# Optimization experiments

Measured on AMD Instinct MI355X. Metric: run time of the kernel, lower is better.

## Reference

```python
import jax, jax.numpy as jnp
import numpy as np

B, S, D = 2, 2048, 7168
R, H, VD = 1024, 16, 128
QK_HD = R // H            # 64, per-head latent q/k dim
SCALE = float(np.sqrt(D // H))  # self.scale = d_heads ** 0.5 = sqrt(448)


def setup_inputs() -> dict:
    key = jax.random.key(0)
    ks = jax.random.split(key, 6)
    return {
        "x":   jax.random.normal(ks[0], (B, S, D), dtype=jnp.float32),
        "Wq":  jax.random.normal(ks[1], (R, D), dtype=jnp.float32) * 0.02,
        "Wkv": jax.random.normal(ks[2], (R, D), dtype=jnp.float32) * 0.02,
        "Wvb": jax.random.normal(ks[3], (H * VD, R), dtype=jnp.float32) * 0.02,
        "Wo":  jax.random.normal(ks[4], (D, H * VD), dtype=jnp.float32) * 0.02,
        "bo":  jnp.zeros((D,), dtype=jnp.float32),
    }


def reference(x, Wq, Wkv, Wvb, Wo, bo):
    b, s, d = x.shape
    # low-rank compressed projections (torch Linear: y = x @ W.T)
    q_lat  = x @ Wq.T            # [B,S,R] compressed query
    kv_lat = x @ Wkv.T           # [B,S,R] compressed KV latent (shared K)
    q = q_lat.reshape(b, s, H, QK_HD)    # [B,S,H,64]
    k = kv_lat.reshape(b, s, H, QK_HD)   # [B,S,H,64]
    # up-project values from latent
    v = (kv_lat @ Wvb.T).reshape(b, s, H, VD)  # [B,S,H,128]
    # scaled causal attention in latent head space
    scores = jnp.einsum("bqhd,bkhd->bhqk", q, k) / SCALE  # [B,H,S,S]
    causal = jnp.tril(jnp.ones((s, s), dtype=bool))
    scores = jnp.where(causal, scores, jnp.finfo(scores.dtype).min)
    attn = jax.nn.softmax(scores, axis=-1)
    out = jnp.einsum("bhqk,bkhd->bqhd", attn, v).reshape(b, s, H * VD)
    return out @ Wo.T + bo       # [B,S,D]
```

## Files before the change

kernel.cpp:

```cpp
#include <hip/hip_runtime.h>
#include <hip/hip_bf16.h>

typedef __bf16 bf16_t;
typedef __attribute__((ext_vector_type(8))) __bf16 bf16x8;
typedef __attribute__((ext_vector_type(4))) __bf16 bf16x4;
typedef __attribute__((ext_vector_type(4))) float f32x4;

#define B_ 2
#define S_ 2048
#define D_ 7168
#define R_ 1024
#define H_ 16
#define VD_ 128
#define MROWS 4096
#define NQKV 2048
#define HVD 2048

__device__ __forceinline__ void gload_lds16(const bf16_t* g, bf16_t* l) {
    __builtin_amdgcn_global_load_lds(
        (const __attribute__((address_space(1))) unsigned int*)(g),
        (__attribute__((address_space(3))) unsigned int*)(l),
        16, 0, 0);
}

__global__ __launch_bounds__(256)
void cvt_fused(const float* __restrict__ x,  const float* __restrict__ Wq,
               const float* __restrict__ Wkv, const float* __restrict__ Wvb,
               const float* __restrict__ Wo,
               bf16_t* __restrict__ xb, bf16_t* __restrict__ Wqkv_b,
               bf16_t* __restrict__ Wvb_b, bf16_t* __restrict__ Wo_b,
               float inv_scale)
{
    const long c = ((long)blockIdx.x * 256 + threadIdx.x);
    const long e = c * 8;
    const float* src; bf16_t* dst; long off; float scale = 1.0f;
    if (e < 29360128L) {
        src = x;   dst = xb;              off = e;
    } else if (e < 36700160L) {
        src = Wq;  dst = Wqkv_b;          off = e - 29360128L; scale = inv_scale;
    } else if (e < 44040192L) {
        src = Wkv; dst = Wqkv_b + 7340032; off = e - 36700160L;
    } else if (e < 46137344L) {
        src = Wvb; dst = Wvb_b;           off = e - 44040192L;
    } else {
        src = Wo;  dst = Wo_b;            off = e - 46137344L;
    }
    f32x4 v0 = *(const f32x4*)(src + off);
    f32x4 v1 = *(const f32x4*)(src + off + 4);
    bf16x8 o;
    o[0] = (bf16_t)(v0[0] * scale); o[1] = (bf16_t)(v0[1] * scale);
    o[2] = (bf16_t)(v0[2] * scale); o[3] = (bf16_t)(v0[3] * scale);
    o[4] = (bf16_t)(v1[0] * scale); o[5] = (bf16_t)(v1[1] * scale);
    o[6] = (bf16_t)(v1[2] * scale); o[7] = (bf16_t)(v1[3] * scale);
    *(bf16x8*)(dst + off) = o;
}

template<int OUTF32>
__global__ __launch_bounds__(256)
void gemm_bt(const bf16_t* __restrict__ A, int lda,
             const bf16_t* __restrict__ Bt, int ldb,
             void* __restrict__ Cv, int ldc,
             const float* __restrict__ bias, int K)
{
    __shared__ __align__(16) bf16_t As[2][128 * 64];
    __shared__ __align__(16) bf16_t Bs[2][128 * 64];
    const int tid  = threadIdx.x;
    const int lane = tid & 63;
    const int wave = tid >> 6;
    const int tileM = blockIdx.y * 128;
    const int tileN = blockIdx.x * 128;
    const int wr = (wave >> 1) * 64;
    const int wc = (wave & 1) * 64;
    const int r  = lane & 15;
    const int kq = lane >> 4;

    const bf16_t* Ag = A  + (size_t)tileM * lda;
    const bf16_t* Bg = Bt + (size_t)tileN * ldb;

    int srow[4], scol[4], slin[4];
    #pragma unroll
    for (int i = 0; i < 4; ++i) {
        slin[i] = (i * 256 + tid) * 8;
        srow[i] = slin[i] >> 6;
        scol[i] = (slin[i] & 63) ^ ((srow[i] & 7) << 3);
    }

    #define ISSUE_TILE(buf, k0)                                                  \
        {                                                                        \
            _Pragma("unroll")                                                    \
            for (int i = 0; i < 4; ++i) {                                        \
                gload_lds16(Ag + (size_t)srow[i] * lda + (k0) + scol[i], As[buf] + slin[i]); \
                gload_lds16(Bg + (size_t)srow[i] * ldb + (k0) + scol[i], Bs[buf] + slin[i]); \
            }                                                                    \
        }

    f32x4 acc[4][4] = {};
    const int nt = K >> 6;

    ISSUE_TILE(0, 0)
    ISSUE_TILE(1, 64)
    asm volatile("s_waitcnt vmcnt(8)" ::: "memory");
    __builtin_amdgcn_s_barrier();
    __builtin_amdgcn_sched_barrier(0);

    for (int t = 0; t < nt; ++t) {
        const int cur = t & 1;
        const bf16_t* Ab = As[cur];
        const bf16_t* Bb = Bs[cur];

        bf16x8 af[4][2], bfr[4][2];
        #pragma unroll
        for (int m = 0; m < 4; ++m)
            #pragma unroll
            for (int kk = 0; kk < 2; ++kk) {
                const int e = (wr + m * 16 + r) * 64 + kk * 32 + kq * 8;
                af[m][kk] = *(const bf16x8*)(Ab + (e ^ ((r & 7) << 3)));
            }
        #pragma unroll
        for (int n = 0; n < 4; ++n)
            #pragma unroll
            for (int kk = 0; kk < 2; ++kk) {
                const int e = (wc + n * 16 + r) * 64 + kk * 32 + kq * 8;
                bfr[n][kk] = *(const bf16x8*)(Bb + (e ^ ((r & 7) << 3)));
            }
        __builtin_amdgcn_s_setprio(1);
        #pragma unroll
        for (int kk = 0; kk < 2; ++kk)
            #pragma unroll
            for (int m = 0; m < 4; ++m)
                #pragma unroll
                for (int n = 0; n < 4; ++n)
                    acc[m][n] = __builtin_amdgcn_mfma_f32_16x16x32_bf16(af[m][kk], bfr[n][kk], acc[m][n], 0, 0, 0);
        __builtin_amdgcn_s_setprio(0);

        __builtin_amdgcn_s_barrier();
        __builtin_amdgcn_sched_barrier(0);
        if (t + 2 < nt) {
            ISSUE_TILE(cur, (t + 2) << 6)
            asm volatile("s_waitcnt vmcnt(8)" ::: "memory");
        } else {
            asm volatile("s_waitcnt vmcnt(0)" ::: "memory");
        }
        __builtin_amdgcn_s_barrier();
        __builtin_amdgcn_sched_barrier(0);
    }
    #undef ISSUE_TILE

    const int orow = tileM + wr + kq * 4;
    const int ocol = tileN + wc + r;
    if (OUTF32) {
        float* C = (float*)Cv;
        #pragma unroll
        for (int n = 0; n < 4; ++n) {
            float bv = bias[ocol + n * 16];
            #pragma unroll
            for (int m = 0; m < 4; ++m)
                #pragma unroll
                for (int j = 0; j < 4; ++j)
                    C[(size_t)(orow + m * 16 + j) * ldc + ocol + n * 16] = acc[m][n][j] + bv;
        }
    } else {
        bf16_t* C = (bf16_t*)Cv;
        #pragma unroll
        for (int m = 0; m < 4; ++m)
            #pragma unroll
            for (int n = 0; n < 4; ++n)
                #pragma unroll
                for (int j = 0; j < 4; ++j)
                    C[(size_t)(orow + m * 16 + j) * ldc + ocol + n * 16] = (bf16_t)acc[m][n][j];
    }
}

template<int OUTF32>
__global__ __launch_bounds__(512, 2)
void gemm_bt256(const bf16_t* __restrict__ A, int lda,
                const bf16_t* __restrict__ Bt, int ldb,
                void* __restrict__ Cv, int ldc,
                const float* __restrict__ bias, int K)
{
    __shared__ __align__(16) bf16_t As[2][256 * 64];
    __shared__ __align__(16) bf16_t Bs[2][256 * 64];
    const int tid  = threadIdx.x;
    const int lane = tid & 63;
    const int wave = tid >> 6;
    const int wm = wave >> 2;
    const int wn = wave & 3;
    const int tileM = blockIdx.y * 256;
    const int tileN = blockIdx.x * 256;
    const int r  = lane & 15;
    const int kq = lane >> 4;

    const bf16_t* Ag = A  + (size_t)tileM * lda;
    const bf16_t* Bg = Bt + (size_t)tileN * ldb;

    int srow[4], scol[4], slin[4];
    #pragma unroll
    for (int i = 0; i < 4; ++i) {
        slin[i] = (i * 512 + tid) * 8;
        srow[i] = slin[i] >> 6;
        scol[i] = (slin[i] & 63) ^ ((srow[i] & 7) << 3);
    }

    #define ISSUE_TILE2(buf, k0)                                                 \
        {                                                                        \
            _Pragma("unroll")                                                    \
            for (int i = 0; i < 4; ++i) {                                        \
                gload_lds16(Ag + (size_t)srow[i] * lda + (k0) + scol[i], As[buf] + slin[i]); \
                gload_lds16(Bg + (size_t)srow[i] * ldb + (k0) + scol[i], Bs[buf] + slin[i]); \
            }                                                                    \
        }

    f32x4 acc[8][4] = {};
    const int nt = K >> 6;

    ISSUE_TILE2(0, 0)
    ISSUE_TILE2(1, 64)
    asm volatile("s_waitcnt vmcnt(8)" ::: "memory");
    __builtin_amdgcn_s_barrier();
    __builtin_amdgcn_sched_barrier(0);

    for (int t = 0; t < nt; ++t) {
        const int cur = t & 1;
        const bf16_t* Ab = As[cur];
        const bf16_t* Bb = Bs[cur];

        {
            bf16x8 af[8], bfr[4];
            #pragma unroll
            for (int m = 0; m < 8; ++m) {
                const int e = (wm * 128 + m * 16 + r) * 64 + kq * 8;
                af[m] = *(const bf16x8*)(Ab + (e ^ ((r & 7) << 3)));
            }
            #pragma unroll
            for (int n = 0; n < 4; ++n) {
                const int e = (wn * 64 + n * 16 + r) * 64 + kq * 8;
                bfr[n] = *(const bf16x8*)(Bb + (e ^ ((r & 7) << 3)));
            }
            __builtin_amdgcn_s_setprio(1);
            #pragma unroll
            for (int m = 0; m < 8; ++m)
                #pragma unroll
                for (int n = 0; n < 4; ++n)
                    acc[m][n] = __builtin_amdgcn_mfma_f32_16x16x32_bf16(af[m], bfr[n], acc[m][n], 0, 0, 0);
            __builtin_amdgcn_s_setprio(0);
        }
        bf16x8 af1[8], bf1[4];
        #pragma unroll
        for (int m = 0; m < 8; ++m) {
            const int e = (wm * 128 + m * 16 + r) * 64 + 32 + kq * 8;
            af1[m] = *(const bf16x8*)(Ab + (e ^ ((r & 7) << 3)));
        }
        #pragma unroll
        for (int n = 0; n < 4; ++n) {
            const int e = (wn * 64 + n * 16 + r) * 64 + 32 + kq * 8;
            bf1[n] = *(const bf16x8*)(Bb + (e ^ ((r & 7) << 3)));
        }
        asm volatile("s_waitcnt lgkmcnt(0)" ::: "memory");
        __builtin_amdgcn_sched_barrier(0);
        __builtin_amdgcn_s_barrier();

        if (t + 2 < nt) { ISSUE_TILE2(cur, (t + 2) << 6) }

        __builtin_amdgcn_s_setprio(1);
        #pragma unroll
        for (int m = 0; m < 8; ++m)
            #pragma unroll
            for (int n = 0; n < 4; ++n)
                acc[m][n] = __builtin_amdgcn_mfma_f32_16x16x32_bf16(af1[m], bf1[n], acc[m][n], 0, 0, 0);
        __builtin_amdgcn_s_setprio(0);

        if (t + 2 < nt) asm volatile("s_waitcnt vmcnt(8)" ::: "memory");
        else            asm volatile("s_waitcnt vmcnt(0)" ::: "memory");
        __builtin_amdgcn_sched_barrier(0);
        __builtin_amdgcn_s_barrier();
        __builtin_amdgcn_sched_barrier(0);
    }
    #undef ISSUE_TILE2

    const int orow = tileM + wm * 128 + kq * 4;
    const int ocol = tileN + wn * 64 + r;
    if (OUTF32) {
        float* C = (float*)Cv;
        #pragma unroll
        for (int n = 0; n < 4; ++n) {
            float bv = bias[ocol + n * 16];
            #pragma unroll
            for (int m = 0; m < 8; ++m)
                #pragma unroll
                for (int j = 0; j < 4; ++j)
                    C[(size_t)(orow + m * 16 + j) * ldc + ocol + n * 16] = acc[m][n][j] + bv;
        }
    } else {
        bf16_t* C = (bf16_t*)Cv;
        #pragma unroll
        for (int m = 0; m < 8; ++m)
            #pragma unroll
            for (int n = 0; n < 4; ++n)
                #pragma unroll
                for (int j = 0; j < 4; ++j)
                    C[(size_t)(orow + m * 16 + j) * ldc + ocol + n * 16] = (bf16_t)acc[m][n][j];
    }
}

__device__ __forceinline__ void attn_qtile(
    const bf16_t* __restrict__ Q, const bf16_t* __restrict__ Kp,
    const bf16_t* __restrict__ Vp, bf16_t* __restrict__ Op,
    bf16_t* __restrict__ P_lds, int qbase, int lane)
{
    const int r  = lane & 15;
    const int kq = lane >> 4;

    bf16x8 qf[2][2];
    #pragma unroll
    for (int m = 0; m < 2; ++m)
        #pragma unroll
        for (int kk = 0; kk < 2; ++kk)
            qf[m][kk] = *(const bf16x8*)(Q + (size_t)(qbase + m * 16 + r) * NQKV + kk * 32 + kq * 8);

    f32x4 o[2][8] = {};
    float mst[2][4], lst[2][4];
    #pragma unroll
    for (int m = 0; m < 2; ++m)
        #pragma unroll
        for (int j = 0; j < 4; ++j) { mst[m][j] = -INFINITY; lst[m][j] = 0.0f; }

    const int nfull  = qbase >> 6;
    const int ntiles = (qbase + 95) >> 6;

    for (int t = 0; t < ntiles; ++t) {
        const int kvb = t * 64;
        f32x4 s[2][4] = {};
        #pragma unroll
        for (int n = 0; n < 4; ++n) {
            bf16x8 kf0 = *(const bf16x8*)(Kp + (size_t)(kvb + n * 16 + r) * NQKV + kq * 8);
            bf16x8 kf1 = *(const bf16x8*)(Kp + (size_t)(kvb + n * 16 + r) * NQKV + 32 + kq * 8);
            #pragma unroll
            for (int m = 0; m < 2; ++m) {
                s[m][n] = __builtin_amdgcn_mfma_f32_16x16x32_bf16(qf[m][0], kf0, s[m][n], 0, 0, 0);
                s[m][n] = __builtin_amdgcn_mfma_f32_16x16x32_bf16(qf[m][1], kf1, s[m][n], 0, 0, 0);
            }
        }
        if (t >= nfull) {
            #pragma unroll
            for (int m = 0; m < 2; ++m)
                #pragma unroll
                for (int n = 0; n < 4; ++n)
                    #pragma unroll
                    for (int j = 0; j < 4; ++j) {
                        int kc = kvb + n * 16 + r;
                        int qr = qbase + m * 16 + kq * 4 + j;
                        if (kc > qr) s[m][n][j] = -1e30f;
                    }
        }
        float mx[2][4];
        #pragma unroll
        for (int m = 0; m < 2; ++m)
            #pragma unroll
            for (int j = 0; j < 4; ++j) {
                float v = fmaxf(fmaxf(s[m][0][j], s[m][1][j]), fmaxf(s[m][2][j], s[m][3][j]));
                #pragma unroll
                for (int d = 1; d < 16; d <<= 1) v = fmaxf(v, __shfl_xor(v, d, 64));
                mx[m][j] = v;
            }
        bool need = false;
        #pragma unroll
        for (int m = 0; m < 2; ++m)
            #pragma unroll
            for (int j = 0; j < 4; ++j) need |= (mx[m][j] > mst[m][j] + 8.0f);
        if (__ballot(need)) {
            #pragma unroll
            for (int m = 0; m < 2; ++m)
                #pragma unroll
                for (int j = 0; j < 4; ++j) {
                    float mnew  = fmaxf(mst[m][j], mx[m][j]);
                    float alpha = __expf(mst[m][j] - mnew);
                    lst[m][j] *= alpha;
                    mst[m][j]  = mnew;
                    #pragma unroll
                    for (int n = 0; n < 8; ++n) o[m][n][j] *= alpha;
                }
        }
        #pragma unroll
        for (int m = 0; m < 2; ++m)
            #pragma unroll
            for (int j = 0; j < 4; ++j) {
                float rs = 0.0f;
                const int row = m * 16 + kq * 4 + j;
                #pragma unroll
                for (int n = 0; n < 4; ++n) {
                    float pv = __expf(s[m][n][j] - mst[m][j]);
                    rs += pv;
                    const int c = (n * 16 + r) ^ ((row & 7) << 3);
                    P_lds[row * 64 + c] = (bf16_t)pv;
                }
                #pragma unroll
                for (int d = 1; d < 16; d <<= 1) rs += __shfl_xor(rs, d, 64);
                lst[m][j] += rs;
            }
        __syncthreads();
        bf16x8 pf[2][2];
        #pragma unroll
        for (int m = 0; m < 2; ++m)
            #pragma unroll
            for (int kk = 0; kk < 2; ++kk) {
                const int e = (m * 16 + r) * 64 + kk * 32 + kq * 8;
                pf[m][kk] = *(const bf16x8*)(P_lds + (e ^ ((r & 7) << 3)));
            }
        #pragma unroll
        for (int n = 0; n < 8; ++n) {
            #pragma unroll
            for (int kk = 0; kk < 2; ++kk) {
                bf16x8 vf = *(const bf16x8*)(Vp + (size_t)(n * 16 + r) * MROWS + kvb + kk * 32 + kq * 8);
                #pragma unroll
                for (int m = 0; m < 2; ++m)
                    o[m][n] = __builtin_amdgcn_mfma_f32_16x16x32_bf16(pf[m][kk], vf, o[m][n], 0, 0, 0);
            }
        }
        __syncthreads();
    }

    #pragma unroll
    for (int m = 0; m < 2; ++m)
        #pragma unroll
        for (int j = 0; j < 4; ++j) {
            float inv = 1.0f / lst[m][j];
            int row = m * 16 + kq * 4 + j;
            #pragma unroll
            for (int n = 0; n < 8; ++n)
                Op[(size_t)(qbase + row) * HVD + n * 16 + r] = (bf16_t)(o[m][n][j] * inv);
        }
}

__global__ __launch_bounds__(64)
void attn_kernel(const bf16_t* __restrict__ qkv, const bf16_t* __restrict__ Vt,
                 bf16_t* __restrict__ O)
{
    __shared__ __align__(16) bf16_t P_lds[32 * 64];
    const int lane = threadIdx.x;
    const int p = blockIdx.x;
    const int h = blockIdx.y;
    const int b = blockIdx.z;

    const bf16_t* Q  = qkv + (size_t)(b * S_) * NQKV + h * 64;
    const bf16_t* Kp = qkv + (size_t)(b * S_) * NQKV + R_ + h * 64;
    const bf16_t* Vp = Vt + (size_t)(h * VD_) * MROWS + b * S_;
    bf16_t* Op = O + (size_t)(b * S_) * HVD + h * VD_;

    attn_qtile(Q, Kp, Vp, Op, P_lds, (63 - p) * 32, lane);
    attn_qtile(Q, Kp, Vp, Op, P_lds, p * 32, lane);
}

extern "C" void kernel_launch(void* const* d_in, const int* in_sizes, int n_in,
                              void* d_out, int out_size, void* d_ws, size_t ws_size,
                              hipStream_t stream) {
    const float* x   = (const float*)d_in[0];
    const float* Wq  = (const float*)d_in[1];
    const float* Wkv = (const float*)d_in[2];
    const float* Wvb = (const float*)d_in[3];
    const float* Wo  = (const float*)d_in[4];
    const float* bo  = (const float*)d_in[5];

    char* oc = (char*)d_out;
    bf16_t* xb     = (bf16_t*)oc;
    bf16_t* Wqkv_b = (bf16_t*)(oc + 58720256);
    char* ws = (char*)d_ws;
    bf16_t* qkv_b  = (bf16_t*)ws;
    bf16_t* Wvb_b  = (bf16_t*)(ws + 16777216);
    bf16_t* Vt_b   = (bf16_t*)(ws + 20971520);
    bf16_t* attn_b = (bf16_t*)(ws + 37748736);
    bf16_t* Wo_b   = (bf16_t*)(ws + 54525952);

    const float inv_scale = 0.047245559f;

    cvt_fused<<<29696, 256, 0, stream>>>(x, Wq, Wkv, Wvb, Wo,
                                         xb, Wqkv_b, Wvb_b, Wo_b, inv_scale);

    gemm_bt<0><<<dim3(16, 32), 256, 0, stream>>>(xb, D_, Wqkv_b, D_, qkv_b, NQKV, nullptr, D_);
    gemm_bt<0><<<dim3(32, 16), 256, 0, stream>>>(Wvb_b, R_, qkv_b + R_, NQKV, Vt_b, MROWS, nullptr, R_);
    attn_kernel<<<dim3(32, H_, B_), 64, 0, stream>>>(qkv_b, Vt_b, attn_b);
    gemm_bt256<1><<<dim3(28, 16), 512, 0, stream>>>(attn_b, HVD, Wo_b, HVD, d_out, D_, bo, HVD);
}
```

Baseline: 487.8 us.

## Restructure output GEMM into 8-phase ping-pong pipeline with split A/B staging

Rewrites the 256x256 output-projection GEMM main loop as eight phases per two K-tiles. Each phase reads a quarter of the A fragments, issues a half-tile of global-to-LDS staging for the next tiles, and runs a small MFMA batch between barriers. The aim is to interleave memory traffic with compute more finely, in the style of ping-pong schedules, so load latency is better hidden. It adds more barriers per tile and relies on intricate vmcnt bookkeeping that could stall or be wrong.

New measurement: 487.8 us, median of 3. Within noise of the previous version (-0.0%).

```diff
diff --git a/kernel.cpp b/kernel.cpp
--- a/kernel.cpp
+++ b/kernel.cpp
@@ -173,10 +173,10 @@
 
 template<int OUTF32>
 __global__ __launch_bounds__(512, 2)
-void gemm_bt256(const bf16_t* __restrict__ A, int lda,
-                const bf16_t* __restrict__ Bt, int ldb,
-                void* __restrict__ Cv, int ldc,
-                const float* __restrict__ bias, int K)
+void gemm_bt256p(const bf16_t* __restrict__ A, int lda,
+                 const bf16_t* __restrict__ Bt, int ldb,
+                 void* __restrict__ Cv, int ldc,
+                 const float* __restrict__ bias, int K)
 {
     __shared__ __align__(16) bf16_t As[2][256 * 64];
     __shared__ __align__(16) bf16_t Bs[2][256 * 64];
@@ -193,89 +193,96 @@
     const bf16_t* Ag = A  + (size_t)tileM * lda;
     const bf16_t* Bg = Bt + (size_t)tileN * ldb;
 
-    int srow[4], scol[4], slin[4];
+    int sr[2], sc[2], sl[2];
     #pragma unroll
-    for (int i = 0; i < 4; ++i) {
-        slin[i] = (i * 512 + tid) * 8;
-        srow[i] = slin[i] >> 6;
-        scol[i] = (slin[i] & 63) ^ ((srow[i] & 7) << 3);
-    }
-
-    #define ISSUE_TILE2(buf, k0)                                                 \
+    for (int i = 0; i < 2; ++i) {
+        sl[i] = (i * 512 + tid) * 8;
+        sr[i] = sl[i] >> 6;
+        sc[i] = (sl[i] & 63) ^ ((sr[i] & 7) << 3);
+    }
+
+    #define STA(buf, k0, h)                                                      \
+        { _Pragma("unroll")                                                      \
+          for (int i = 0; i < 2; ++i)                                            \
+              gload_lds16(Ag + (size_t)((h) * 128 + sr[i]) * lda + (k0) + sc[i], \
+                          As[buf] + (h) * 8192 + sl[i]); }
+    #define STB(buf, k0, h)                                                      \
+        { _Pragma("unroll")                                                      \
+          for (int i = 0; i < 2; ++i)                                            \
+              gload_lds16(Bg + (size_t)((h) * 128 + sr[i]) * ldb + (k0) + sc[i], \
+                          Bs[buf] + (h) * 8192 + sl[i]); }
+
+    #define PHASE(buf, q, READB, STAGE_STMT, VM_STMT)                            \
         {                                                                        \
+            const bf16_t* Ab_ = As[buf];                                         \
+            const bf16_t* Bb_ = Bs[buf];                                         \
+            bf16x8 af_[2][2];                                                    \
             _Pragma("unroll")                                                    \
-            for (int i = 0; i < 4; ++i) {                                        \
-                gload_lds16(Ag + (size_t)srow[i] * lda + (k0) + scol[i], As[buf] + slin[i]); \
-                gload_lds16(Bg + (size_t)srow[i] * ldb + (k0) + scol[i], Bs[buf] + slin[i]); \
+            for (int mm = 0; mm < 2; ++mm)                                       \
+                _Pragma("unroll")                                                \
+                for (int kk = 0; kk < 2; ++kk) {                                 \
+                    const int e = (wm * 128 + ((q) * 2 + mm) * 16 + r) * 64 + kk * 32 + kq * 8; \
+                    af_[mm][kk] = *(const bf16x8*)(Ab_ + (e ^ ((r & 7) << 3)));  \
+                }                                                                \
+            if (READB) {                                                         \
+                _Pragma("unroll")                                                \
+                for (int n = 0; n < 4; ++n)                                      \
+                    _Pragma("unroll")                                            \
+                    for (int kk = 0; kk < 2; ++kk) {                             \
+                        const int e = (wn * 64 + n * 16 + r) * 64 + kk * 32 + kq * 8; \
+                        bf[n][kk] = *(const bf16x8*)(Bb_ + (e ^ ((r & 7) << 3))); \
+                    }                                                            \
             }                                                                    \
+            STAGE_STMT                                                           \
+            VM_STMT                                                              \
+            __builtin_amdgcn_s_barrier();                                        \
+            asm volatile("s_waitcnt lgkmcnt(0)" ::: "memory");                   \
+            __builtin_amdgcn_sched_barrier(0);                                   \
+            __builtin_amdgcn_s_setprio(1);                                       \
+            _Pragma("unroll")                                                    \
+            for (int mm = 0; mm < 2; ++mm)                                       \
+                _Pragma("unroll")                                                \
+                for (int n = 0; n < 4; ++n)                                      \
+                    _Pragma("unroll")                                            \
+                    for (int kk = 0; kk < 2; ++kk)                               \
+                        acc[(q) * 2 + mm][n] = __builtin_amdgcn_mfma_f32_16x16x32_bf16( \
+                            af_[mm][kk], bf[n][kk], acc[(q) * 2 + mm][n], 0, 0, 0); \
+            __builtin_amdgcn_s_setprio(0);                                       \
+            __builtin_amdgcn_s_barrier();                                        \
+            __builtin_amdgcn_sched_barrier(0);                                   \
         }
 
     f32x4 acc[8][4] = {};
     const int nt = K >> 6;
-
-    ISSUE_TILE2(0, 0)
-    ISSUE_TILE2(1, 64)
-    asm volatile("s_waitcnt vmcnt(8)" ::: "memory");
+    const int niter = nt >> 1;
+
+    STA(0, 0, 0) STA(0, 0, 1) STB(0, 0, 0) STB(0, 0, 1) STB(1, 64, 0) STB(1, 64, 1)
+    asm volatile("s_waitcnt vmcnt(4)" ::: "memory");
     __builtin_amdgcn_s_barrier();
     __builtin_amdgcn_sched_barrier(0);
 
-    for (int t = 0; t < nt; ++t) {
-        const int cur = t & 1;
-        const bf16_t* Ab = As[cur];
-        const bf16_t* Bb = Bs[cur];
-
-        {
-            bf16x8 af[8], bfr[4];
-            #pragma unroll
-            for (int m = 0; m < 8; ++m) {
-                const int e = (wm * 128 + m * 16 + r) * 64 + kq * 8;
-                af[m] = *(const bf16x8*)(Ab + (e ^ ((r & 7) << 3)));
-            }
-            #pragma unroll
-            for (int n = 0; n < 4; ++n) {
-                const int e = (wn * 64 + n * 16 + r) * 64 + kq * 8;
-                bfr[n] = *(const bf16x8*)(Bb + (e ^ ((r & 7) << 3)));
-            }
-            __builtin_amdgcn_s_setprio(1);
-            #pragma unroll
-            for (int m = 0; m < 8; ++m)
-                #pragma unroll
-                for (int n = 0; n < 4; ++n)
-                    acc[m][n] = __builtin_amdgcn_mfma_f32_16x16x32_bf16(af[m], bfr[n], acc[m][n], 0, 0, 0);
-            __builtin_amdgcn_s_setprio(0);
-        }
-        bf16x8 af1[8], bf1[4];
-        #pragma unroll
-        for (int m = 0; m < 8; ++m) {
-            const int e = (wm * 128 + m * 16 + r) * 64 + 32 + kq * 8;
-            af1[m] = *(const bf16x8*)(Ab + (e ^ ((r & 7) << 3)));
-        }
-        #pragma unroll
-        for (int n = 0; n < 4; ++n) {
-            const int e = (wn * 64 + n * 16 + r) * 64 + 32 + kq * 8;
-            bf1[n] = *(const bf16x8*)(Bb + (e ^ ((r & 7) << 3)));
-        }
-        asm volatile("s_waitcnt lgkmcnt(0)" ::: "memory");
-        __builtin_amdgcn_sched_barrier(0);
-        __builtin_amdgcn_s_barrier();
-
-        if (t + 2 < nt) { ISSUE_TILE2(cur, (t + 2) << 6) }
-
-        __builtin_amdgcn_s_setprio(1);
-        #pragma unroll
-        for (int m = 0; m < 8; ++m)
-            #pragma unroll
-            for (int n = 0; n < 4; ++n)
-                acc[m][n] = __builtin_amdgcn_mfma_f32_16x16x32_bf16(af1[m], bf1[n], acc[m][n], 0, 0, 0);
-        __builtin_amdgcn_s_setprio(0);
-
-        if (t + 2 < nt) asm volatile("s_waitcnt vmcnt(8)" ::: "memory");
-        else            asm volatile("s_waitcnt vmcnt(0)" ::: "memory");
-        __builtin_amdgcn_sched_barrier(0);
-        __builtin_amdgcn_s_barrier();
-        __builtin_amdgcn_sched_barrier(0);
-    }
-    #undef ISSUE_TILE2
+    for (int t = 0; t < niter; ++t) {
+        const int k1 = (2 * t + 1) << 6;
+        const int k2 = (2 * t + 2) << 6;
+        const int k3 = (2 * t + 3) << 6;
+        const bool more = (2 * t + 2) < nt;
+        bf16x8 bf[4][2];
+
+        PHASE(0, 0, 1, { STA(1, k1, 0) }, {})
+        PHASE(0, 1, 0, { STA(1, k1, 1) }, {})
+        PHASE(0, 2, 0, { if (more) STB(0, k2, 0) }, {})
+        PHASE(0, 3, 0, { if (more) STB(0, k2, 1) },
+              { if (more) { asm volatile("s_waitcnt vmcnt(4)" ::: "memory"); }
+                else      { asm volatile("s_waitcnt vmcnt(0)" ::: "memory"); } })
+        PHASE(1, 0, 1, { if (more) STA(0, k2, 0) }, {})
+        PHASE(1, 1, 0, { if (more) STA(0, k2, 1) }, {})
+        PHASE(1, 2, 0, { if (more) STB(1, k3, 0) }, {})
+        PHASE(1, 3, 0, { if (more) STB(1, k3, 1) },
+              { if (more) { asm volatile("s_waitcnt vmcnt(4)" ::: "memory"); } })
+    }
+    #undef PHASE
+    #undef STA
+    #undef STB
 
     const int orow = tileM + wm * 128 + kq * 4;
     const int ocol = tileN + wn * 64 + r;
@@ -478,5 +485,5 @@
     gemm_bt<0><<<dim3(16, 32), 256, 0, stream>>>(xb, D_, Wqkv_b, D_, qkv_b, NQKV, nullptr, D_);
     gemm_bt<0><<<dim3(32, 16), 256, 0, stream>>>(Wvb_b, R_, qkv_b + R_, NQKV, Vt_b, MROWS, nullptr, R_);
     attn_kernel<<<dim3(32, H_, B_), 64, 0, stream>>>(qkv_b, Vt_b, attn_b);
-    gemm_bt256<1><<<dim3(28, 16), 512, 0, stream>>>(attn_b, HVD, Wo_b, HVD, d_out, D_, bo, HVD);
-}
+    gemm_bt256p<1><<<dim3(28, 16), 512, 0, stream>>>(attn_b, HVD, Wo_b, HVD, d_out, D_, bo, HVD);
+}
```
